# Kernel optimization log

Hardware: AMD Instinct MI355X
Metric: run time of the kernel (lower is better)

The kernel has to match this reference:

```python
import jax, jax.numpy as jnp
import numpy as np

RADIUS = 4.0

def _gather(x, idx):
    # x: [b, C, N], idx: [b, n, k] -> out: [b, C, k, n]
    b, C, N = x.shape
    _, n, k = idx.shape
    idxT = jnp.broadcast_to(idx.transpose(0, 2, 1)[:, None, :, :], (b, C, k, n))
    return jnp.take_along_axis(x[:, :, None, :], idxT, axis=3)


def setup_inputs() -> dict:
    key = jax.random.key(0)
    k1, k2, k3, k4, k5, k6 = jax.random.split(key, 6)
    b, N, k = 2, 50000, 16
    c_in, c_out, K = 64, 128, 5
    c2 = c_out // 2
    xyz = jax.random.normal(k1, (b, 3, N), dtype=jnp.float32)
    fea = jax.random.normal(k2, (b, c_in, N), dtype=jnp.float32)
    knn_idx = jax.random.randint(k3, (b, N, k), 0, N)
    conv_w = jax.random.normal(k4, (c2, c_in), dtype=jnp.float32) * 0.05
    conv_b = jax.random.normal(k5, (c2,), dtype=jnp.float32) * 0.01
    # uniform init matching torch: bound = sqrt(3)*gain/sqrt(fan), gain=sqrt(2), fan=16
    bound = float(np.sqrt(3.0) * np.sqrt(2.0) / np.sqrt(16.0))
    conv_dw = jax.random.uniform(k6, (1, c2, K, K, K), dtype=jnp.float32, minval=-bound, maxval=bound)
    return {"xyz": xyz, "fea": fea, "knn_idx": knn_idx, "conv_w": conv_w, "conv_b": conv_b, "conv_dw": conv_dw}


def reference(xyz, fea, knn_idx, conv_w, conv_b, conv_dw):
    b, n, k = knn_idx.shape
    K = conv_dw.shape[-1]
    # --- geometry: gather neighbor coords, relative coords, normalize ---
    neighbor_xyz = _gather(xyz, knn_idx)            # [b, 3, k, n]
    rel = neighbor_xyz - xyz[:, :, None, :]         # [b, 3, k, n]
    std = jnp.std(rel, axis=(2, 3), keepdims=True, ddof=1)  # torch unbiased std
    sample = rel / (RADIUS * std)                   # normalized grid coords in channel dim
    # --- features: residual gather (center + neighbor diffs), 1x1 conv ---
    center = fea[:, :, None, :]                     # [b, C, 1, n]
    nb = _gather(fea, knn_idx[:, :, 1:])            # [b, C, k-1, n]
    nfea = jnp.concatenate([center, nb - center], axis=2)  # [b, C, k, n]
    nfea = jnp.einsum('oc,bckn->bokn', conv_w, nfea) + conv_b[None, :, None, None]
    # --- grid_sample(mode='nearest', padding='border', align_corners=False) ---
    def to_idx(coord):
        ix = ((coord + 1.0) * K - 1.0) * 0.5
        return jnp.clip(jnp.round(ix), 0, K - 1).astype(jnp.int32)
    ix = to_idx(sample[:, 0])  # grid x -> W index, [b, k, n]
    iy = to_idx(sample[:, 1])  # grid y -> H index
    iz = to_idx(sample[:, 2])  # grid z -> D index
    kern = conv_dw[0][:, iz, iy, ix]                # [C2, b, k, n]
    kern = jnp.transpose(kern, (1, 0, 2, 3))        # [b, C2, k, n]
    # --- weighted reduce over neighbors + mean branch ---
    out = jnp.concatenate([(kern * nfea).sum(axis=2), nfea.mean(axis=2)], axis=1)
    return out  # [b, out_channels, n]
```

## Files before the change

kernel.cpp:

```cpp
#include <hip/hip_runtime.h>
#include <hip/hip_bf16.h>
#include <math.h>

#define NPTS 50000
#define BATCH 2
#define CIN 64
#define C2 64
#define KNN 16
#define NCELL 125
#define MTOT 800000


using bf16x8 = __attribute__((ext_vector_type(8))) short;
using f32x4  = __attribute__((ext_vector_type(4))) float;
using f32x2  = __attribute__((ext_vector_type(2))) float;

__device__ __forceinline__ float bflo(unsigned int v) { return __uint_as_float(v << 16); }
__device__ __forceinline__ float bfhi(unsigned int v) { return __uint_as_float(v & 0xffff0000u); }
__device__ __forceinline__ f32x2 unpk(unsigned int v) {
    f32x2 r;
    r.x = __uint_as_float(v << 16);
    r.y = __uint_as_float(v & 0xffff0000u);
    return r;
}
__device__ __forceinline__ unsigned short f2bf(float f) {
    __hip_bfloat16 h = __float2bfloat16(f);
    return *(unsigned short*)&h;
}

__device__ __forceinline__ int to_cell32(float s) {
    float x = __fmul_rn(__fsub_rn(__fmul_rn(__fadd_rn(s, 1.0f), 5.0f), 1.0f), 0.5f);
    x = rintf(x);
    x = fminf(fmaxf(x, 0.0f), 4.0f);
    return (int)x;
}

__device__ __forceinline__ void leafwalk(int l, int& off, int& n) {
    off = 0; n = 25000;
    #pragma unroll
    for (int d = 7; d >= 0; --d) {
        int n2 = (n >> 1); n2 -= (n2 & 7);
        if ((l >> d) & 1) { off += n2; n -= n2; } else { n = n2; }
    }
}

__global__ __launch_bounds__(256) void kfuse1(const float* __restrict__ xyz,
                                              const int* __restrict__ knn,
                                              const float* __restrict__ fea,
                                              const float* __restrict__ W,
                                              unsigned short* __restrict__ g,
                                              float* __restrict__ relc0,
                                              float* __restrict__ wsf) {
    __shared__ unsigned short flds[64 * 72];
    int bx = blockIdx.x;
    int t = threadIdx.x;
    if (bx < 1564) {
        int b = (bx >= 782);
        int tile = bx - b * 782;
        int n0 = tile * 64;
        int nrem = NPTS - n0; if (nrem > 64) nrem = 64;
        const float* fb = fea + (size_t)b * CIN * NPTS;
        int j = t & 63, w = t >> 6;
        int lane = t & 63, li = lane & 15, gq = lane >> 4;
        #pragma unroll
        for (int i = 0; i < 8; ++i) {
            int c = w * 2 + i * 8;
            float v0 = (j < nrem) ? fb[(size_t)c * NPTS + n0 + j] : 0.0f;
            float v1 = (j < nrem) ? fb[(size_t)(c + 1) * NPTS + n0 + j] : 0.0f;
            unsigned int pk = (unsigned int)f2bf(v0) | ((unsigned int)f2bf(v1) << 16);
            *(unsigned int*)&flds[j * 72 + c] = pk;
        }
        bf16x8 af[4][2];
        #pragma unroll
        for (int mt = 0; mt < 4; ++mt)
            #pragma unroll
            for (int kh = 0; kh < 2; ++kh) {
                const float* wp = W + (mt * 16 + li) * CIN + kh * 32 + gq * 8;
                float4 wa = *(const float4*)wp;
                float4 wb = *(const float4*)(wp + 4);
                bf16x8 a;
                a[0] = (short)f2bf(wa.x); a[1] = (short)f2bf(wa.y);
                a[2] = (short)f2bf(wa.z); a[3] = (short)f2bf(wa.w);
                a[4] = (short)f2bf(wb.x); a[5] = (short)f2bf(wb.y);
                a[6] = (short)f2bf(wb.z); a[7] = (short)f2bf(wb.w);
                af[mt][kh] = a;
            }
        __syncthreads();
        f32x4 acc[4];
        #pragma unroll
        for (int mt = 0; mt < 4; ++mt) acc[mt] = (f32x4){0.f, 0.f, 0.f, 0.f};
        #pragma unroll
        for (int kh = 0; kh < 2; ++kh) {
            bf16x8 bfv = *(const bf16x8*)&flds[(w * 16 + li) * 72 + kh * 32 + gq * 8];
            #pragma unroll
            for (int mt = 0; mt < 4; ++mt)
                acc[mt] = __builtin_amdgcn_mfma_f32_16x16x32_bf16(af[mt][kh], bfv,
                                                                  acc[mt], 0, 0, 0);
        }
        int nloc = w * 16 + li;
        if (nloc < nrem) {
            unsigned short* gr = g + ((size_t)b * NPTS + n0 + nloc) * C2;
            #pragma unroll
            for (int mt = 0; mt < 4; ++mt) {
                int ob = mt * 16 + gq * 4;
                uint2 pk;
                pk.x = (unsigned int)f2bf(acc[mt][0]) | ((unsigned int)f2bf(acc[mt][1]) << 16);
                pk.y = (unsigned int)f2bf(acc[mt][2]) | ((unsigned int)f2bf(acc[mt][3]) << 16);
                *(uint2*)(gr + ob) = pk;
            }
        }
    } else {
        float* lsum = (float*)flds;
        int pid = bx - 1564;
        int b = pid >> 8, r8 = pid & 255;
        int s = r8 >> 3, blk = r8 & 7;
        const float* xb = xyz + (size_t)b * 3 * NPTS;
        const int* kb = knn + (size_t)b * NPTS * KNN;
        float* relc = relc0 + (size_t)b * 3 * MTOT;
        int l = blk * 32 + (t >> 3);
        int j = t & 7;
        int off, n;
        leafwalk(l, off, n);
        int base = s * 25000 + off;
        float r0 = 0.0f, r1 = 0.0f, r2 = 0.0f;
        int i = j;
        for (; i + 24 < n; i += 32) {
            int f0 = base + i, f1 = f0 + 8, f2 = f0 + 16, f3 = f0 + 24;
            int kk0 = f0 / NPTS, nn0 = f0 - kk0 * NPTS;
            int kk1 = f1 / NPTS, nn1 = f1 - kk1 * NPTS;
            int kk2 = f2 / NPTS, nn2 = f2 - kk2 * NPTS;
            int kk3 = f3 / NPTS, nn3 = f3 - kk3 * NPTS;
            int jA = kb[nn0 * KNN + kk0];
            int jB = kb[nn1 * KNN + kk1];
            int jC = kb[nn2 * KNN + kk2];
            int jD = kb[nn3 * KNN + kk3];
            float vA0 = __fsub_rn(xb[jA],            xb[nn0]);
            float vA1 = __fsub_rn(xb[NPTS + jA],     xb[NPTS + nn0]);
            float vA2 = __fsub_rn(xb[2 * NPTS + jA], xb[2 * NPTS + nn0]);
            float vB0 = __fsub_rn(xb[jB],            xb[nn1]);
            float vB1 = __fsub_rn(xb[NPTS + jB],     xb[NPTS + nn1]);
            float vB2 = __fsub_rn(xb[2 * NPTS + jB], xb[2 * NPTS + nn1]);
            float vC0 = __fsub_rn(xb[jC],            xb[nn2]);
            float vC1 = __fsub_rn(xb[NPTS + jC],     xb[NPTS + nn2]);
            float vC2 = __fsub_rn(xb[2 * NPTS + jC], xb[2 * NPTS + nn2]);
            float vD0 = __fsub_rn(xb[jD],            xb[nn3]);
            float vD1 = __fsub_rn(xb[NPTS + jD],     xb[NPTS + nn3]);
            float vD2 = __fsub_rn(xb[2 * NPTS + jD], xb[2 * NPTS + nn3]);
            relc[f0] = vA0; relc[MTOT + f0] = vA1; relc[2 * MTOT + f0] = vA2;
            relc[f1] = vB0; relc[MTOT + f1] = vB1; relc[2 * MTOT + f1] = vB2;
            relc[f2] = vC0; relc[MTOT + f2] = vC1; relc[2 * MTOT + f2] = vC2;
            relc[f3] = vD0; relc[MTOT + f3] = vD1; relc[2 * MTOT + f3] = vD2;
            r0 = __fadd_rn(r0, vA0); r1 = __fadd_rn(r1, vA1); r2 = __fadd_rn(r2, vA2);
            r0 = __fadd_rn(r0, vB0); r1 = __fadd_rn(r1, vB1); r2 = __fadd_rn(r2, vB2);
            r0 = __fadd_rn(r0, vC0); r1 = __fadd_rn(r1, vC1); r2 = __fadd_rn(r2, vC2);
            r0 = __fadd_rn(r0, vD0); r1 = __fadd_rn(r1, vD1); r2 = __fadd_rn(r2, vD2);
        }
        for (; i < n; i += 8) {
            int f = base + i;
            int kk = f / NPTS, nn = f - kk * NPTS;
            int jj = kb[nn * KNN + kk];
            float v0 = __fsub_rn(xb[jj],            xb[nn]);
            float v1 = __fsub_rn(xb[NPTS + jj],     xb[NPTS + nn]);
            float v2 = __fsub_rn(xb[2 * NPTS + jj], xb[2 * NPTS + nn]);
            relc[f] = v0; relc[MTOT + f] = v1; relc[2 * MTOT + f] = v2;
            r0 = __fadd_rn(r0, v0); r1 = __fadd_rn(r1, v1); r2 = __fadd_rn(r2, v2);
        }
        float a0 = __fadd_rn(r0, __shfl_xor(r0, 1));
        a0 = __fadd_rn(a0, __shfl_xor(a0, 2));
        a0 = __fadd_rn(a0, __shfl_xor(a0, 4));
        float a1 = __fadd_rn(r1, __shfl_xor(r1, 1));
        a1 = __fadd_rn(a1, __shfl_xor(a1, 2));
        a1 = __fadd_rn(a1, __shfl_xor(a1, 4));
        float a2 = __fadd_rn(r2, __shfl_xor(r2, 1));
        a2 = __fadd_rn(a2, __shfl_xor(a2, 2));
        a2 = __fadd_rn(a2, __shfl_xor(a2, 4));
        #pragma unroll
        for (int c = 0; c < 3; ++c) {
            float rc = (c == 0) ? a0 : ((c == 1) ? a1 : a2);
            __syncthreads();
            if (j == 0) lsum[t >> 3] = rc;
            __syncthreads();
            for (int m = 16; m >= 1; m >>= 1) {
                float v = 0.0f;
                if (t < m) v = __fadd_rn(lsum[2 * t], lsum[2 * t + 1]);
                __syncthreads();
                if (t < m) lsum[t] = v;
                __syncthreads();
            }
            if (t == 0) wsf[16 + ((size_t)(b * 3 + c) * 32 + s) * 8 + blk] = lsum[0];
        }
    }
}

__global__ __launch_bounds__(256) void kfuse2(const float* __restrict__ dw,
                                              const float* __restrict__ relc0,
                                              float* __restrict__ wsf) {
    __shared__ float lsum[34];
    int bx = blockIdx.x;
    int t = threadIdx.x;
    if (bx < 1536) {
        int pid = bx;
        int b = pid / 768, rem = pid - b * 768;
        int c = rem >> 8, r8 = rem & 255;
        int s = r8 >> 3, blk = r8 & 7;

        const float* P = wsf + 16 + (size_t)(b * 3 + c) * 256;
        if (t < 32) {
            const float* q = P + t * 8;
            float a  = __fadd_rn(__fadd_rn(q[0], q[1]), __fadd_rn(q[2], q[3]));
            float b2 = __fadd_rn(__fadd_rn(q[4], q[5]), __fadd_rn(q[6], q[7]));
            lsum[t] = __fadd_rn(a, b2);
        }
        __syncthreads();
        for (int m = 16; m >= 1; m >>= 1) {
            float v = 0.0f;
            if (t < m) v = __fadd_rn(lsum[2 * t], lsum[2 * t + 1]);
            __syncthreads();
            if (t < m) lsum[t] = v;
            __syncthreads();
        }
        if (t == 0) lsum[33] = lsum[0] / 800000.0f;
        __syncthreads();
        float mean = lsum[33];
        __syncthreads();

        const float* relc = relc0 + (size_t)(b * 3 + c) * MTOT;
        int l = blk * 32 + (t >> 3);
        int j = t & 7;
        int off, n;
        leafwalk(l, off, n);
        int base = s * 25000 + off;
        float r = 0.0f;
        int i = j;
        for (; i + 24 < n; i += 32) {
            float a0 = relc[base + i];
            float a1 = relc[base + i + 8];
            float a2 = relc[base + i + 16];
            float a3 = relc[base + i + 24];
            float d0 = __fsub_rn(a0, mean);
            float d1 = __fsub_rn(a1, mean);
            float d2 = __fsub_rn(a2, mean);
            float d3 = __fsub_rn(a3, mean);
            r = __fadd_rn(r, __fmul_rn(d0, d0));
            r = __fadd_rn(r, __fmul_rn(d1, d1));
            r = __fadd_rn(r, __fmul_rn(d2, d2));
            r = __fadd_rn(r, __fmul_rn(d3, d3));
        }
        for (; i < n; i += 8) {
            float d0 = __fsub_rn(relc[base + i], mean);
            r = __fadd_rn(r, __fmul_rn(d0, d0));
        }
        float a = __fadd_rn(r, __shfl_xor(r, 1));
        a = __fadd_rn(a, __shfl_xor(a, 2));
        a = __fadd_rn(a, __shfl_xor(a, 4));
        if (j == 0) lsum[t >> 3] = a;
        __syncthreads();
        for (int m = 16; m >= 1; m >>= 1) {
            float v = 0.0f;
            if (t < m) v = __fadd_rn(lsum[2 * t], lsum[2 * t + 1]);
            __syncthreads();
            if (t < m) lsum[t] = v;
            __syncthreads();
        }
        if (t == 0) wsf[2048 + ((size_t)(b * 3 + c) * 32 + s) * 8 + blk] = lsum[0];
    } else {
        unsigned int* gdwp = (unsigned int*)(wsf + 8192);
        int i0 = (bx - 1536) * 250;
        for (int i = i0 + t; i < i0 + 250; i += 256) {
            int cell = i >> 5, u = i & 31;
            unsigned int p0 = f2bf(dw[(2 * u)     * NCELL + cell]);
            unsigned int p1 = f2bf(dw[(2 * u + 1) * NCELL + cell]);
            gdwp[i] = p0 | (p1 << 16);
        }
    }
}

__global__ __launch_bounds__(256, 6) void kmain(const float* __restrict__ xyz,
                                                const int* __restrict__ idx,
                                                const float* __restrict__ cb,
                                                const unsigned short* __restrict__ g,
                                                const float* __restrict__ wsf,
                                                float* __restrict__ out) {
    __shared__ unsigned int  dwp[NCELL * 32];
    __shared__ unsigned char celllds[64 * KNN];
    __shared__ float         ctr[3][64];
    __shared__ float         res[128 * 17];
    int bx = blockIdx.x;
    int b = (bx >= 782);
    int n0 = (bx - b * 782) * 64;
    int t = threadIdx.x;
    int nrem = NPTS - n0; if (nrem > 64) nrem = 64;

    float* l3 = res;
    if (t < 96) {
        int c = t >> 5, l = t & 31;
        const float* q = wsf + 2048 + (size_t)(b * 3 + c) * 256 + l * 8;
        float a  = __fadd_rn(__fadd_rn(q[0], q[1]), __fadd_rn(q[2], q[3]));
        float b2 = __fadd_rn(__fadd_rn(q[4], q[5]), __fadd_rn(q[6], q[7]));
        l3[c * 32 + l] = __fadd_rn(a, b2);
    }
    __syncthreads();
    for (int m = 16; m >= 1; m >>= 1) {
        float v = 0.0f;
        int c = t >> 5, l = t & 31;
        if (t < 96 && l < m) v = __fadd_rn(l3[c * 32 + 2 * l], l3[c * 32 + 2 * l + 1]);
        __syncthreads();
        if (t < 96 && l < m) l3[c * 32 + l] = v;
        __syncthreads();
    }
    float dn0 = __fmul_rn(4.0f, sqrtf(l3[0]  / 799999.0f));
    float dn1 = __fmul_rn(4.0f, sqrtf(l3[32] / 799999.0f));
    float dn2 = __fmul_rn(4.0f, sqrtf(l3[64] / 799999.0f));
    __syncthreads();

    const unsigned int* gdwp = (const unsigned int*)(wsf + 8192);
    for (int i = t; i < NCELL * 32; i += 256) dwp[i] = gdwp[i];
    const float* xb = xyz + (size_t)b * 3 * NPTS;
    if (t < 192) {
        int c = t >> 6, jx = t & 63;
        if (jx < nrem) ctr[c][jx] = xb[c * NPTS + n0 + jx];
    }
    const int* ib = idx + ((size_t)b * NPTS + n0) * KNN;
    __syncthreads();

    for (int i = t; i < nrem * KNN; i += 256) {
        int p = i >> 4;
        int jx = ib[i];
        float sx = __fsub_rn(xb[jx],            ctr[0][p]) / dn0;
        float sy = __fsub_rn(xb[NPTS + jx],     ctr[1][p]) / dn1;
        float sz = __fsub_rn(xb[2 * NPTS + jx], ctr[2][p]) / dn2;
        celllds[i] = (unsigned char)((to_cell32(sz) * 5 + to_cell32(sy)) * 5 + to_cell32(sx));
    }
    __syncthreads();

    int w = t >> 6, h = (t >> 5) & 1, u = t & 31;
    int o0 = 2 * u, o1 = 2 * u + 1;
    f32x2 cbv;
    cbv.x = cb[o0]; cbv.y = cb[o1];
    const unsigned short* gbp = g + (size_t)b * NPTS * C2;
    float* ob = out + (size_t)b * 128 * NPTS;

    #pragma unroll 1
    for (int chunk = 0; chunk < 4; ++chunk) {
        int pbase = chunk * 16;
        #pragma unroll 1
        for (int i = 0; i < 2; ++i) {
            int p = pbase + i * 8 + w * 2 + h;
            if (p < nrem) {
                const int* row = ib + p * KNN;
                unsigned int gnu = *(const unsigned int*)(gbp + (size_t)(n0 + p) * C2 + o0);
                unsigned int gvv[15];
                #pragma unroll
                for (int k = 0; k < 15; ++k) {
                    int jj = row[k + 1];
                    gvv[k] = *(const unsigned int*)(gbp + (size_t)jj * C2 + o0);
                }
                int cell0 = celllds[p * KNN];
                f32x2 k0v = unpk(dwp[cell0 * 32 + u]);
                f32x2 gn  = unpk(gnu);
                f32x2 ws = {0.f, 0.f}, gs = {0.f, 0.f}, sk = {0.f, 0.f};
                #pragma unroll
                for (int k = 0; k < 15; ++k) {
                    int cell = celllds[p * KNN + k + 1];
                    f32x2 dp = unpk(dwp[cell * 32 + u]);
                    f32x2 gv = unpk(gvv[k]);
                    ws += dp * gv;
                    gs += gv;
                    sk += dp;
                }
                f32x2 r1 = cbv * (k0v + sk) + gn * (k0v - sk) + ws;
                f32x2 r2 = cbv + 0.0625f * (gs - 14.0f * gn);
                int pl = p & 15;
                res[o0 * 17 + pl]        = r1.x;
                res[o1 * 17 + pl]        = r1.y;
                res[(64 + o0) * 17 + pl] = r2.x;
                res[(64 + o1) * 17 + pl] = r2.y;
            }
        }
        __syncthreads();
        int rl = t >> 4;
        int jn = t & 15;
        int ncol = nrem - pbase; if (ncol > 16) ncol = 16;
        if (jn < ncol) {
            for (int r2 = rl; r2 < 128; r2 += 16)
                ob[(size_t)r2 * NPTS + n0 + pbase + jn] = res[r2 * 17 + jn];
        }
        __syncthreads();
    }
}

extern "C" void kernel_launch(void* const* d_in, const int* in_sizes, int n_in,
                              void* d_out, int out_size, void* d_ws, size_t ws_size,
                              hipStream_t stream) {
    const float* xyz   = (const float*)d_in[0];
    const float* fea   = (const float*)d_in[1];
    const int*   knn   = (const int*)d_in[2];
    const float* convw = (const float*)d_in[3];
    const float* convb = (const float*)d_in[4];
    const float* convdw= (const float*)d_in[5];
    float* out = (float*)d_out;
    float* wsf = (float*)d_ws;
    unsigned short* g = (unsigned short*)(wsf + 16384);
    float* relc = out;

    kfuse1<<<1564 + 512, 256, 0, stream>>>(xyz, knn, fea, convw, g, relc, wsf);
    kfuse2<<<1536 + 16, 256, 0, stream>>>(convdw, relc, wsf);
    kmain <<<782 * 2, 256, 0, stream>>>(xyz, knn, convb, g, wsf, out);
}
```

Baseline: 120.1 us.

## Transpose xyz to AoS float3 and fuse per-channel variance passes

Adds a prep kernel that transposes xyz into an interleaved float3 array in workspace and packs the depthwise kernel weights to bf16, which moves that packing out of the old second kernel. The relative-coordinate gathers in kfuse1 and kmain now fetch one float3 per point instead of three strided floats, and relative coordinates are stored as float3 records. The variance kernel handles all three channels in one pass over the float3 buffer rather than launching separate blocks per channel. The cost is an extra kernel launch and an extra pass over xyz.

Result: faster. 102.8 us (-14.4%).

```diff
diff --git a/kernel.cpp b/kernel.cpp
--- a/kernel.cpp
+++ b/kernel.cpp
@@ -15,8 +15,6 @@
 using f32x4  = __attribute__((ext_vector_type(4))) float;
 using f32x2  = __attribute__((ext_vector_type(2))) float;
 
-__device__ __forceinline__ float bflo(unsigned int v) { return __uint_as_float(v << 16); }
-__device__ __forceinline__ float bfhi(unsigned int v) { return __uint_as_float(v & 0xffff0000u); }
 __device__ __forceinline__ f32x2 unpk(unsigned int v) {
     f32x2 r;
     r.x = __uint_as_float(v << 16);
@@ -44,12 +42,38 @@
     }
 }
 
-__global__ __launch_bounds__(256) void kfuse1(const float* __restrict__ xyz,
-                                              const int* __restrict__ knn,
+__global__ __launch_bounds__(256) void kprep(const float* __restrict__ xyz,
+                                             const float* __restrict__ dw,
+                                             float* __restrict__ wsf) {
+    int bx = blockIdx.x;
+    int t = threadIdx.x;
+    if (bx < 391) {
+        int gid = bx * 256 + t;
+        if (gid < 2 * NPTS) {
+            int b = (gid >= NPTS);
+            int n = gid - b * NPTS;
+            const float* xb = xyz + (size_t)b * 3 * NPTS;
+            float3 v;
+            v.x = xb[n]; v.y = xb[NPTS + n]; v.z = xb[2 * NPTS + n];
+            ((float3*)(wsf + 16384))[gid] = v;
+        }
+    } else {
+        unsigned int* gdwp = (unsigned int*)(wsf + 8192);
+        int i0 = (bx - 391) * 250;
+        for (int i = i0 + t; i < i0 + 250; i += 256) {
+            int cell = i >> 5, u = i & 31;
+            unsigned int p0 = f2bf(dw[(2 * u)     * NCELL + cell]);
+            unsigned int p1 = f2bf(dw[(2 * u + 1) * NCELL + cell]);
+            gdwp[i] = p0 | (p1 << 16);
+        }
+    }
+}
+
+__global__ __launch_bounds__(256) void kfuse1(const int* __restrict__ knn,
                                               const float* __restrict__ fea,
                                               const float* __restrict__ W,
                                               unsigned short* __restrict__ g,
-                                              float* __restrict__ relc0,
+                                              float3* __restrict__ rel3,
                                               float* __restrict__ wsf) {
     __shared__ unsigned short flds[64 * 72];
     int bx = blockIdx.x;
@@ -111,12 +135,13 @@
         }
     } else {
         float* lsum = (float*)flds;
+        const float3* xyzT = (const float3*)(wsf + 16384);
         int pid = bx - 1564;
         int b = pid >> 8, r8 = pid & 255;
         int s = r8 >> 3, blk = r8 & 7;
-        const float* xb = xyz + (size_t)b * 3 * NPTS;
+        const float3* xT = xyzT + (size_t)b * NPTS;
         const int* kb = knn + (size_t)b * NPTS * KNN;
-        float* relc = relc0 + (size_t)b * 3 * MTOT;
+        float3* relb = rel3 + (size_t)b * MTOT;
         int l = blk * 32 + (t >> 3);
         int j = t & 7;
         int off, n;
@@ -134,36 +159,30 @@
             int jB = kb[nn1 * KNN + kk1];
             int jC = kb[nn2 * KNN + kk2];
             int jD = kb[nn3 * KNN + kk3];
-            float vA0 = __fsub_rn(xb[jA],            xb[nn0]);
-            float vA1 = __fsub_rn(xb[NPTS + jA],     xb[NPTS + nn0]);
-            float vA2 = __fsub_rn(xb[2 * NPTS + jA], xb[2 * NPTS + nn0]);
-            float vB0 = __fsub_rn(xb[jB],            xb[nn1]);
-            float vB1 = __fsub_rn(xb[NPTS + jB],     xb[NPTS + nn1]);
-            float vB2 = __fsub_rn(xb[2 * NPTS + jB], xb[2 * NPTS + nn1]);
-            float vC0 = __fsub_rn(xb[jC],            xb[nn2]);
-            float vC1 = __fsub_rn(xb[NPTS + jC],     xb[NPTS + nn2]);
-            float vC2 = __fsub_rn(xb[2 * NPTS + jC], xb[2 * NPTS + nn2]);
-            float vD0 = __fsub_rn(xb[jD],            xb[nn3]);
-            float vD1 = __fsub_rn(xb[NPTS + jD],     xb[NPTS + nn3]);
-            float vD2 = __fsub_rn(xb[2 * NPTS + jD], xb[2 * NPTS + nn3]);
-            relc[f0] = vA0; relc[MTOT + f0] = vA1; relc[2 * MTOT + f0] = vA2;
-            relc[f1] = vB0; relc[MTOT + f1] = vB1; relc[2 * MTOT + f1] = vB2;
-            relc[f2] = vC0; relc[MTOT + f2] = vC1; relc[2 * MTOT + f2] = vC2;
-            relc[f3] = vD0; relc[MTOT + f3] = vD1; relc[2 * MTOT + f3] = vD2;
-            r0 = __fadd_rn(r0, vA0); r1 = __fadd_rn(r1, vA1); r2 = __fadd_rn(r2, vA2);
-            r0 = __fadd_rn(r0, vB0); r1 = __fadd_rn(r1, vB1); r2 = __fadd_rn(r2, vB2);
-            r0 = __fadd_rn(r0, vC0); r1 = __fadd_rn(r1, vC1); r2 = __fadd_rn(r2, vC2);
-            r0 = __fadd_rn(r0, vD0); r1 = __fadd_rn(r1, vD1); r2 = __fadd_rn(r2, vD2);
+            float3 cA = xT[nn0], nA = xT[jA];
+            float3 cB = xT[nn1], nB = xT[jB];
+            float3 cC = xT[nn2], nC = xT[jC];
+            float3 cD = xT[nn3], nD = xT[jD];
+            float3 vA, vB, vC, vD;
+            vA.x = __fsub_rn(nA.x, cA.x); vA.y = __fsub_rn(nA.y, cA.y); vA.z = __fsub_rn(nA.z, cA.z);
+            vB.x = __fsub_rn(nB.x, cB.x); vB.y = __fsub_rn(nB.y, cB.y); vB.z = __fsub_rn(nB.z, cB.z);
+            vC.x = __fsub_rn(nC.x, cC.x); vC.y = __fsub_rn(nC.y, cC.y); vC.z = __fsub_rn(nC.z, cC.z);
+            vD.x = __fsub_rn(nD.x, cD.x); vD.y = __fsub_rn(nD.y, cD.y); vD.z = __fsub_rn(nD.z, cD.z);
+            relb[f0] = vA; relb[f1] = vB; relb[f2] = vC; relb[f3] = vD;
+            r0 = __fadd_rn(r0, vA.x); r1 = __fadd_rn(r1, vA.y); r2 = __fadd_rn(r2, vA.z);
+            r0 = __fadd_rn(r0, vB.x); r1 = __fadd_rn(r1, vB.y); r2 = __fadd_rn(r2, vB.z);
+            r0 = __fadd_rn(r0, vC.x); r1 = __fadd_rn(r1, vC.y); r2 = __fadd_rn(r2, vC.z);
+            r0 = __fadd_rn(r0, vD.x); r1 = __fadd_rn(r1, vD.y); r2 = __fadd_rn(r2, vD.z);
         }
         for (; i < n; i += 8) {
             int f = base + i;
             int kk = f / NPTS, nn = f - kk * NPTS;
             int jj = kb[nn * KNN + kk];
-            float v0 = __fsub_rn(xb[jj],            xb[nn]);
-            float v1 = __fsub_rn(xb[NPTS + jj],     xb[NPTS + nn]);
-            float v2 = __fsub_rn(xb[2 * NPTS + jj], xb[2 * NPTS + nn]);
-            relc[f] = v0; relc[MTOT + f] = v1; relc[2 * MTOT + f] = v2;
-            r0 = __fadd_rn(r0, v0); r1 = __fadd_rn(r1, v1); r2 = __fadd_rn(r2, v2);
+            float3 cc = xT[nn], nv = xT[jj];
+            float3 v;
+            v.x = __fsub_rn(nv.x, cc.x); v.y = __fsub_rn(nv.y, cc.y); v.z = __fsub_rn(nv.z, cc.z);
+            relb[f] = v;
+            r0 = __fadd_rn(r0, v.x); r1 = __fadd_rn(r1, v.y); r2 = __fadd_rn(r2, v.z);
         }
         float a0 = __fadd_rn(r0, __shfl_xor(r0, 1));
         a0 = __fadd_rn(a0, __shfl_xor(a0, 2));
@@ -192,86 +211,95 @@
     }
 }
 
-__global__ __launch_bounds__(256) void kfuse2(const float* __restrict__ dw,
-                                              const float* __restrict__ relc0,
-                                              float* __restrict__ wsf) {
-    __shared__ float lsum[34];
-    int bx = blockIdx.x;
+__global__ __launch_bounds__(256) void kpw2(const float3* __restrict__ rel3,
+                                            float* __restrict__ wsf) {
+    __shared__ float sm[96];
+    int r8 = blockIdx.x;
+    int s = r8 >> 3, blk = r8 & 7;
+    int b = blockIdx.y;
     int t = threadIdx.x;
-    if (bx < 1536) {
-        int pid = bx;
-        int b = pid / 768, rem = pid - b * 768;
-        int c = rem >> 8, r8 = rem & 255;
-        int s = r8 >> 3, blk = r8 & 7;
-
-        const float* P = wsf + 16 + (size_t)(b * 3 + c) * 256;
-        if (t < 32) {
-            const float* q = P + t * 8;
-            float a  = __fadd_rn(__fadd_rn(q[0], q[1]), __fadd_rn(q[2], q[3]));
-            float b2 = __fadd_rn(__fadd_rn(q[4], q[5]), __fadd_rn(q[6], q[7]));
-            lsum[t] = __fadd_rn(a, b2);
-        }
+
+    if (t < 96) {
+        int c = t >> 5, l = t & 31;
+        const float* q = wsf + 16 + (size_t)(b * 3 + c) * 256 + l * 8;
+        float a  = __fadd_rn(__fadd_rn(q[0], q[1]), __fadd_rn(q[2], q[3]));
+        float b2 = __fadd_rn(__fadd_rn(q[4], q[5]), __fadd_rn(q[6], q[7]));
+        sm[c * 32 + l] = __fadd_rn(a, b2);
+    }
+    __syncthreads();
+    for (int m = 16; m >= 1; m >>= 1) {
+        float v = 0.0f;
+        int c = t >> 5, l = t & 31;
+        if (t < 96 && l < m) v = __fadd_rn(sm[c * 32 + 2 * l], sm[c * 32 + 2 * l + 1]);
+        __syncthreads();
+        if (t < 96 && l < m) sm[c * 32 + l] = v;
+        __syncthreads();
+    }
+    float m0 = sm[0]  / 800000.0f;
+    float m1 = sm[32] / 800000.0f;
+    float m2 = sm[64] / 800000.0f;
+    __syncthreads();
+
+    const float3* relb = rel3 + (size_t)b * MTOT;
+    int l = blk * 32 + (t >> 3);
+    int j = t & 7;
+    int off, n;
+    leafwalk(l, off, n);
+    int base = s * 25000 + off;
+    float r0 = 0.0f, r1 = 0.0f, r2 = 0.0f;
+    int i = j;
+    for (; i + 24 < n; i += 32) {
+        float3 vA = relb[base + i];
+        float3 vB = relb[base + i + 8];
+        float3 vC = relb[base + i + 16];
+        float3 vD = relb[base + i + 24];
+        float dA0 = __fsub_rn(vA.x, m0), dA1 = __fsub_rn(vA.y, m1), dA2 = __fsub_rn(vA.z, m2);
+        float dB0 = __fsub_rn(vB.x, m0), dB1 = __fsub_rn(vB.y, m1), dB2 = __fsub_rn(vB.z, m2);
+        float dC0 = __fsub_rn(vC.x, m0), dC1 = __fsub_rn(vC.y, m1), dC2 = __fsub_rn(vC.z, m2);
+        float dD0 = __fsub_rn(vD.x, m0), dD1 = __fsub_rn(vD.y, m1), dD2 = __fsub_rn(vD.z, m2);
+        r0 = __fadd_rn(r0, __fmul_rn(dA0, dA0));
+        r1 = __fadd_rn(r1, __fmul_rn(dA1, dA1));
+        r2 = __fadd_rn(r2, __fmul_rn(dA2, dA2));
+        r0 = __fadd_rn(r0, __fmul_rn(dB0, dB0));
+        r1 = __fadd_rn(r1, __fmul_rn(dB1, dB1));
+        r2 = __fadd_rn(r2, __fmul_rn(dB2, dB2));
+        r0 = __fadd_rn(r0, __fmul_rn(dC0, dC0));
+        r1 = __fadd_rn(r1, __fmul_rn(dC1, dC1));
+        r2 = __fadd_rn(r2, __fmul_rn(dC2, dC2));
+        r0 = __fadd_rn(r0, __fmul_rn(dD0, dD0));
+        r1 = __fadd_rn(r1, __fmul_rn(dD1, dD1));
+        r2 = __fadd_rn(r2, __fmul_rn(dD2, dD2));
+    }
+    for (; i < n; i += 8) {
+        float3 v = relb[base + i];
+        float d0 = __fsub_rn(v.x, m0), d1 = __fsub_rn(v.y, m1), d2 = __fsub_rn(v.z, m2);
+        r0 = __fadd_rn(r0, __fmul_rn(d0, d0));
+        r1 = __fadd_rn(r1, __fmul_rn(d1, d1));
+        r2 = __fadd_rn(r2, __fmul_rn(d2, d2));
+    }
+    float a0 = __fadd_rn(r0, __shfl_xor(r0, 1));
+    a0 = __fadd_rn(a0, __shfl_xor(a0, 2));
+    a0 = __fadd_rn(a0, __shfl_xor(a0, 4));
+    float a1 = __fadd_rn(r1, __shfl_xor(r1, 1));
+    a1 = __fadd_rn(a1, __shfl_xor(a1, 2));
+    a1 = __fadd_rn(a1, __shfl_xor(a1, 4));
+    float a2 = __fadd_rn(r2, __shfl_xor(r2, 1));
+    a2 = __fadd_rn(a2, __shfl_xor(a2, 2));
+    a2 = __fadd_rn(a2, __shfl_xor(a2, 4));
+    #pragma unroll
+    for (int c = 0; c < 3; ++c) {
+        float rc = (c == 0) ? a0 : ((c == 1) ? a1 : a2);
+        __syncthreads();
+        if (j == 0) sm[t >> 3] = rc;
         __syncthreads();
         for (int m = 16; m >= 1; m >>= 1) {
             float v = 0.0f;
-            if (t < m) v = __fadd_rn(lsum[2 * t], lsum[2 * t + 1]);
+            if (t < m) v = __fadd_rn(sm[2 * t], sm[2 * t + 1]);
             __syncthreads();
-            if (t < m) lsum[t] = v;
+            if (t < m) sm[t] = v;
             __syncthreads();
         }
-        if (t == 0) lsum[33] = lsum[0] / 800000.0f;
-        __syncthreads();
-        float mean = lsum[33];
-        __syncthreads();
-
-        const float* relc = relc0 + (size_t)(b * 3 + c) * MTOT;
-        int l = blk * 32 + (t >> 3);
-        int j = t & 7;
-        int off, n;
-        leafwalk(l, off, n);
-        int base = s * 25000 + off;
-        float r = 0.0f;
-        int i = j;
-        for (; i + 24 < n; i += 32) {
-            float a0 = relc[base + i];
-            float a1 = relc[base + i + 8];
-            float a2 = relc[base + i + 16];
-            float a3 = relc[base + i + 24];
-            float d0 = __fsub_rn(a0, mean);
-            float d1 = __fsub_rn(a1, mean);
-            float d2 = __fsub_rn(a2, mean);
-            float d3 = __fsub_rn(a3, mean);
-            r = __fadd_rn(r, __fmul_rn(d0, d0));
-            r = __fadd_rn(r, __fmul_rn(d1, d1));
-            r = __fadd_rn(r, __fmul_rn(d2, d2));
-            r = __fadd_rn(r, __fmul_rn(d3, d3));
-        }
-        for (; i < n; i += 8) {
-            float d0 = __fsub_rn(relc[base + i], mean);
-            r = __fadd_rn(r, __fmul_rn(d0, d0));
-        }
-        float a = __fadd_rn(r, __shfl_xor(r, 1));
-        a = __fadd_rn(a, __shfl_xor(a, 2));
-        a = __fadd_rn(a, __shfl_xor(a, 4));
-        if (j == 0) lsum[t >> 3] = a;
-        __syncthreads();
-        for (int m = 16; m >= 1; m >>= 1) {
-            float v = 0.0f;
-            if (t < m) v = __fadd_rn(lsum[2 * t], lsum[2 * t + 1]);
-            __syncthreads();
-            if (t < m) lsum[t] = v;
-            __syncthreads();
-        }
-        if (t == 0) wsf[2048 + ((size_t)(b * 3 + c) * 32 + s) * 8 + blk] = lsum[0];
-    } else {
-        unsigned int* gdwp = (unsigned int*)(wsf + 8192);
-        int i0 = (bx - 1536) * 250;
-        for (int i = i0 + t; i < i0 + 250; i += 256) {
-            int cell = i >> 5, u = i & 31;
-            unsigned int p0 = f2bf(dw[(2 * u)     * NCELL + cell]);
-            unsigned int p1 = f2bf(dw[(2 * u + 1) * NCELL + cell]);
-            gdwp[i] = p0 | (p1 << 16);
-        }
+        if (t == 0) wsf[2048 + ((size_t)(b * 3 + c) * 32 + s) * 8 + blk] = sm[0];
     }
 }
 
@@ -316,6 +344,7 @@
     const unsigned int* gdwp = (const unsigned int*)(wsf + 8192);
     for (int i = t; i < NCELL * 32; i += 256) dwp[i] = gdwp[i];
     const float* xb = xyz + (size_t)b * 3 * NPTS;
+    const float3* xT = (const float3*)(wsf + 16384) + (size_t)b * NPTS;
     if (t < 192) {
         int c = t >> 6, jx = t & 63;
         if (jx < nrem) ctr[c][jx] = xb[c * NPTS + n0 + jx];
@@ -326,9 +355,10 @@
     for (int i = t; i < nrem * KNN; i += 256) {
         int p = i >> 4;
         int jx = ib[i];
-        float sx = __fsub_rn(xb[jx],            ctr[0][p]) / dn0;
-        float sy = __fsub_rn(xb[NPTS + jx],     ctr[1][p]) / dn1;
-        float sz = __fsub_rn(xb[2 * NPTS + jx], ctr[2][p]) / dn2;
+        float3 pj = xT[jx];
+        float sx = __fsub_rn(pj.x, ctr[0][p]) / dn0;
+        float sy = __fsub_rn(pj.y, ctr[1][p]) / dn1;
+        float sz = __fsub_rn(pj.z, ctr[2][p]) / dn2;
         celllds[i] = (unsigned char)((to_cell32(sz) * 5 + to_cell32(sy)) * 5 + to_cell32(sx));
     }
     __syncthreads();
@@ -400,10 +430,11 @@
     const float* convdw= (const float*)d_in[5];
     float* out = (float*)d_out;
     float* wsf = (float*)d_ws;
-    unsigned short* g = (unsigned short*)(wsf + 16384);
-    float* relc = out;
-
-    kfuse1<<<1564 + 512, 256, 0, stream>>>(xyz, knn, fea, convw, g, relc, wsf);
-    kfuse2<<<1536 + 16, 256, 0, stream>>>(convdw, relc, wsf);
+    unsigned short* g = (unsigned short*)(wsf + 327680);
+    float3* rel3 = (float3*)out;
+
+    kprep <<<407, 256, 0, stream>>>(xyz, convdw, wsf);
+    kfuse1<<<1564 + 512, 256, 0, stream>>>(knn, fea, convw, g, rel3, wsf);
+    kpw2  <<<dim3(256, BATCH), 256, 0, stream>>>(rel3, wsf);
     kmain <<<782 * 2, 256, 0, stream>>>(xyz, knn, convb, g, wsf, out);
 }
```
